# Kernel optimization log

Hardware: AMD Instinct MI355X
Metric: run time of the kernel (lower is better)

## Reference

```python
import jax, jax.numpy as jnp
import numpy as np

N = 100000      # hits
K = 256         # max truth objects per event
C = 2           # n_ccoords
NCLS = 6        # n_classes
Q_MIN = 0.5
S_B = 1.0
ENERGY_DEN_OFFSET = 1.0
PAYLOAD_BETA_CLIP = 0.1
USE_AVG_CC = 0.0
BETA_CLIP = 1.0 - 1e-5


def _divide_no_nan(num, den):
    return jnp.where(den == 0.0, 0.0, num / jnp.where(den == 0.0, 1.0, den))


def setup_inputs() -> dict:
    key = jax.random.key(0)
    ks = jax.random.split(key, 12)
    pred_beta = jax.random.uniform(ks[0], (N, 1), minval=0.01, maxval=0.99)
    pred_ccoords = jax.random.normal(ks[1], (N, C))
    pred_energy = jax.random.uniform(ks[2], (N, 1), minval=0.0, maxval=100.0)
    pred_pos = 50.0 * jax.random.normal(ks[3], (N, 2))
    pred_time = jax.random.normal(ks[4], (N, 1))
    pred_id = jax.random.normal(ks[5], (N, NCLS))
    t_energy = jax.random.uniform(ks[6], (N, 1), minval=0.1, maxval=100.0)
    t_pos = 50.0 * jax.random.normal(ks[7], (N, 2))
    t_time = jax.random.normal(ks[8], (N, 1))
    t_pid = jax.random.randint(ks[9], (N, 1), 1, NCLS + 1).astype(jnp.float32)
    t_idx = jax.random.randint(ks[10], (N, 1), -1, K)  # -1 == noise
    rowsplits = jnp.array([0, N], dtype=jnp.int32)
    return dict(pred_beta=pred_beta, pred_ccoords=pred_ccoords,
                pred_energy=pred_energy, pred_pos=pred_pos,
                pred_time=pred_time, pred_id=pred_id,
                t_energy=t_energy, t_pos=t_pos, t_time=t_time, t_pid=t_pid,
                t_idx=t_idx, rowsplits=rowsplits)


def oc_loss(pred_beta, pred_ccoords, pred_energy, pred_pos, pred_time,
            pred_id, t_energy, t_pos, t_time, t_pid, t_idx):
    beta = jnp.clip(pred_beta[:, 0], 0.0, BETA_CLIP)          # [N]
    q = jnp.arctanh(beta) ** 2 + Q_MIN                        # [N] charge
    tidx = t_idx[:, 0]
    not_noise = tidx >= 0                                     # [N]
    tclip = jnp.where(not_noise, tidx, 0)

    # hit->object assignment matrix [N, K]
    M = jax.nn.one_hot(tclip, K, dtype=beta.dtype) * not_noise[:, None].astype(beta.dtype)
    counts = M.sum(axis=0)                                    # [K]
    obj_valid = counts > 0.0
    n_valid = jnp.maximum(obj_valid.sum().astype(beta.dtype), 1.0)

    # condensation point per object: highest-beta hit of that object
    score = jnp.where(M > 0.0, beta[:, None], -1.0)           # [N, K]
    alpha = jnp.argmax(score, axis=0)                         # [K]
    x_alpha = pred_ccoords[alpha]                             # [K, C]
    mean_cc = (M.T @ pred_ccoords) / jnp.maximum(counts, 1.0)[:, None]
    x_k = USE_AVG_CC * mean_cc + (1.0 - USE_AVG_CC) * x_alpha
    q_alpha = q[alpha]                                        # [K]
    beta_alpha = beta[alpha]

    # pairwise hit <-> condensation-point squared distances [N, K]
    diff = pred_ccoords[:, None, :] - x_k[None, :, :]
    distsq = jnp.sum(diff * diff, axis=-1)

    qq = q[:, None] * q_alpha[None, :]                        # [N, K]
    # attractive potential: own-object hits pulled toward condensation point
    v_att_k = (M * distsq * qq).sum(axis=0) / jnp.maximum(counts, 1.0)
    V_att = jnp.where(obj_valid, v_att_k, 0.0).sum() / n_valid
    # repulsive potential: all other hits pushed out of a unit ball
    hinge = jax.nn.relu(1.0 - jnp.sqrt(distsq + 1e-6))
    v_rep_k = ((1.0 - M) * hinge * qq).sum(axis=0) / jnp.maximum(N - counts, 1.0)
    V_rep = jnp.where(obj_valid, v_rep_k, 0.0).sum() / n_valid

    # beta terms: sharpen condensation points, suppress noise beta
    L_beta = jnp.where(obj_valid, 1.0 - beta_alpha, 0.0).sum() / n_valid
    n_noise = jnp.maximum((~not_noise).astype(beta.dtype).sum(), 1.0)
    L_noise = S_B * jnp.where(not_noise, 0.0, beta).sum() / n_noise

    # --- per-hit payload losses ---
    ew = jax.nn.relu(jnp.where(t_energy > 10.0,
                               1.0, (t_energy - 0.5) / 10.0 * 10.0 / 9.5))
    e_loss = _divide_no_nan((t_energy - pred_energy) ** 2,
                            t_energy + ENERGY_DEN_OFFSET)
    p_loss = jnp.sum((t_pos - pred_pos) ** 2, axis=-1, keepdims=True) / 100.0
    tm_loss = (t_time - pred_time) ** 2
    cls_loss = 1e-8 * jnp.mean(pred_id ** 2, axis=-1, keepdims=True)
    payload = jnp.concatenate([e_loss, p_loss, tm_loss, cls_loss], axis=-1) * ew  # [N,4]
    payload = jnp.where(pred_beta < PAYLOAD_BETA_CLIP, 0.0, payload)

    # beta-weighted average of payload over each truth object
    pw = beta * not_noise.astype(beta.dtype)                  # [N]
    num = M.T @ (payload * pw[:, None])                       # [K, 4]
    den = (M * pw[:, None]).sum(axis=0)                       # [K]
    per_obj = num / jnp.maximum(den, 1e-6)[:, None]
    L_payload = (jnp.where(obj_valid[:, None], per_obj, 0.0).sum(axis=0) / n_valid).sum()

    return V_att + V_rep + L_beta + L_noise + L_payload


def reference(pred_beta, pred_ccoords, pred_energy, pred_pos, pred_time,
              pred_id, t_energy, t_pos, t_time, t_pid, t_idx, rowsplits):
    return oc_loss(pred_beta, pred_ccoords, pred_energy, pred_pos, pred_time,
                   pred_id, t_energy, t_pos, t_time, t_pid, t_idx)
```

## Files before the change

kernel.cpp:

```cpp
#include <hip/hip_runtime.h>
#include <hip/hip_bf16.h>
#include <math.h>

#define KOBJ 256
#define B1   256
#define NW   4
#define WSTR 257
#define QMIN 0.5f
#define BETA_CLIP_C (1.0f - 1e-5f)

typedef unsigned long long u64;

__global__ __launch_bounds__(256) void partials(
    const float*  __restrict__ pred_beta,
    const float*  __restrict__ pred_energy,
    const float2* __restrict__ pred_pos,
    const float*  __restrict__ pred_time,
    const float2* __restrict__ pred_id2,
    const float*  __restrict__ t_energy,
    const float2* __restrict__ t_pos,
    const float*  __restrict__ t_time,
    const int*    __restrict__ t_idx,
    u64*    __restrict__ pk_part,
    float*  __restrict__ cnt_part,
    float*  __restrict__ den_part,
    float*  __restrict__ num_part,
    float*  __restrict__ noise_part,
    int n)
{
    __shared__ u64   spk[NW][WSTR];
    __shared__ float scnt[NW][WSTR], sden[NW][WSTR], snum[NW][WSTR];
    __shared__ float snoise[256];
    int t = threadIdx.x;
    int b = blockIdx.x;
    int w = t >> 6;
    for (int i = t; i < NW * WSTR; i += 256) {
        ((u64*)spk)[i] = 0;
        ((float*)scnt)[i] = 0.f;
        ((float*)sden)[i] = 0.f;
        ((float*)snum)[i] = 0.f;
    }
    __syncthreads();

    float noise = 0.0f;
    for (int i = b * 256 + t; i < n; i += B1 * 256) {
        int tid = t_idx[i];
        float braw = pred_beta[i];
        float beta = fminf(fmaxf(braw, 0.0f), BETA_CLIP_C);
        if (tid >= 0) {
            atomicAdd(&scnt[w][tid], 1.0f);
            u64 key = ((u64)__float_as_uint(beta) << 32) |
                      (u64)(0x7FFFFFFFu - (unsigned)i);
            atomicMax(&spk[w][tid], key);
            float te = t_energy[i];
            float ew = (te > 10.0f) ? 1.0f : fmaxf(0.0f, (te - 0.5f) / 9.5f);
            float de = te - pred_energy[i];
            float el = de * de / (te + 1.0f);
            float2 tp = t_pos[i];
            float2 pp = pred_pos[i];
            float dpx = tp.x - pp.x, dpy = tp.y - pp.y;
            float pl = (dpx * dpx + dpy * dpy) * 0.01f;
            float dt = t_time[i] - pred_time[i];
            float tl = dt * dt;
            float2 id0 = pred_id2[3 * i];
            float2 id1 = pred_id2[3 * i + 1];
            float2 id2 = pred_id2[3 * i + 2];
            float cs = id0.x * id0.x + id0.y * id0.y + id1.x * id1.x +
                       id1.y * id1.y + id2.x * id2.x + id2.y * id2.y;
            cs *= (1e-8f / 6.0f);
            float mask = (braw < 0.1f) ? 0.0f : 1.0f;
            float wgt = mask * ew * beta;
            atomicAdd(&sden[w][tid], beta);
            atomicAdd(&snum[w][tid], (el + pl + tl + cs) * wgt);
        } else {
            noise += beta;
        }
    }
    __syncthreads();
    u64 pk = spk[0][t];
    { u64 q = spk[1][t]; if (q > pk) pk = q; }
    { u64 q = spk[2][t]; if (q > pk) pk = q; }
    { u64 q = spk[3][t]; if (q > pk) pk = q; }
    float cnt = scnt[0][t] + scnt[1][t] + scnt[2][t] + scnt[3][t];
    float den = sden[0][t] + sden[1][t] + sden[2][t] + sden[3][t];
    float num = snum[0][t] + snum[1][t] + snum[2][t] + snum[3][t];
    int o = t * B1 + b;
    pk_part[o]  = pk;
    cnt_part[o] = cnt;
    den_part[o] = den;
    num_part[o] = num;
    snoise[t] = noise;
    __syncthreads();
    for (int s = 128; s > 0; s >>= 1) {
        if (t < s) snoise[t] += snoise[t + s];
        __syncthreads();
    }
    if (t == 0) noise_part[b] = snoise[0];
}

__global__ __launch_bounds__(256) void merge(
    const float2* __restrict__ pred_ccoords,
    const u64*    __restrict__ pk_part,
    const float*  __restrict__ cnt_part,
    const float*  __restrict__ den_part,
    const float*  __restrict__ num_part,
    float4* __restrict__ objA,
    float4* __restrict__ objB)
{
    __shared__ u64   spk[256];
    __shared__ float scnt[256], sden[256], snum[256];
    int k = blockIdx.x;
    int b = threadIdx.x;
    int o = k * B1 + b;
    u64 pk = pk_part[o];
    float cnt = cnt_part[o];
    float den = den_part[o];
    float nsum = num_part[o];
    spk[b] = pk; scnt[b] = cnt; sden[b] = den; snum[b] = nsum;
    __syncthreads();
    for (int s = 128; s > 0; s >>= 1) {
        if (b < s) {
            u64 p = spk[b + s]; if (p > spk[b]) spk[b] = p;
            scnt[b] += scnt[b + s];
            sden[b] += sden[b + s];
            snum[b] += snum[b + s];
        }
        __syncthreads();
    }
    if (b == 0) {
        float cs = scnt[0];
        bool valid = cs > 0.f;
        float xk = 0.f, yk = 0.f, qa = 0.f, lb = 0.f, pay = 0.f;
        if (valid) {
            u64 p = spk[0];
            unsigned a = 0x7FFFFFFFu - (unsigned)(p & 0xFFFFFFFFull);
            float ba = __uint_as_float((unsigned)(p >> 32));
            float2 cc = pred_ccoords[a];
            xk = cc.x; yk = cc.y;
            float at = atanhf(ba);
            qa = at * at + QMIN;
            lb = 1.0f - ba;
            pay = snum[0] / fmaxf(sden[0], 1e-6f);
        }
        objA[k] = make_float4(xk, yk, qa, cs);
        objB[k] = make_float4(pay, lb, valid ? 1.f : 0.f, 0.f);
    }
}

__global__ __launch_bounds__(256) void heavy(
    const float*  __restrict__ pred_beta,
    const float2* __restrict__ pred_ccoords,
    const int*    __restrict__ t_idx,
    const float4* __restrict__ objA,
    float* __restrict__ rep_part,
    float* __restrict__ att_part,
    int n, int hstr)
{
    __shared__ float4 pts[256];
    int t = threadIdx.x;
    int p = blockIdx.x * 256 + t;
    float4 pt;
    if (p < n) {
        float beta = fminf(fmaxf(pred_beta[p], 0.0f), BETA_CLIP_C);
        float at = atanhf(beta);
        float2 cc = pred_ccoords[p];
        pt = make_float4(cc.x, cc.y, at * at + QMIN, __int_as_float(t_idx[p]));
    } else {
        pt = make_float4(0.f, 0.f, 0.f, __int_as_float(-2));
    }
    pts[t] = pt;
    float4 oa = objA[t];
    float xk = oa.x, yk = oa.y;
    __syncthreads();
    float rep = 0.f, att = 0.f;
    #pragma unroll 8
    for (int j = 0; j < 256; ++j) {
        float4 s = pts[j];
        float dx = s.x - xk, dy = s.y - yk;
        float d2 = fmaf(dy, dy, fmaf(dx, dx, 1e-6f));
        float r = __builtin_amdgcn_sqrtf(d2);
        float h = fmaxf(0.0f, 1.0f - r);
        bool own = (__float_as_int(s.w) == t);
        rep = fmaf(own ? 0.0f : h,  s.z, rep);
        att = fmaf(own ? d2 : 0.0f, s.z, att);
    }
    int o = t * hstr + blockIdx.x;
    rep_part[o] = rep;
    att_part[o] = att;
}

__global__ __launch_bounds__(256) void final1(
    const float4* __restrict__ objA,
    const float4* __restrict__ objB,
    const float*  __restrict__ rep_part,
    const float*  __restrict__ att_part,
    float4* __restrict__ objC,
    int n, int nbh, int hstr)
{
    __shared__ float srep[256], satt[256];
    int k = blockIdx.x;
    int b = threadIdx.x;
    float rep = 0.f, att = 0.f;
    int o = k * hstr + b;
    if (b < nbh)        { rep += rep_part[o];        att += att_part[o]; }
    if (b + 256 < nbh)  { rep += rep_part[o + 256];  att += att_part[o + 256]; }
    srep[b] = rep; satt[b] = att;
    __syncthreads();
    for (int s = 128; s > 0; s >>= 1) {
        if (b < s) { srep[b] += srep[b + s]; satt[b] += satt[b + s]; }
        __syncthreads();
    }
    if (b == 0) {
        float4 a  = objA[k];
        float4 b4 = objB[k];
        float cnt = a.w, qa = a.z, valid = b4.z;
        float vatt = valid * satt[0] * qa / fmaxf(cnt, 1.0f);
        float vrep = valid * srep[0] * qa / fmaxf((float)n - cnt, 1.0f);
        objC[k] = make_float4(vatt + vrep + b4.y + b4.x, valid, cnt, 0.f);
    }
}

__global__ __launch_bounds__(256) void final2(
    const float4* __restrict__ objC,
    const float*  __restrict__ noise_part,
    float* __restrict__ out, int n)
{
    __shared__ float4 sred[256];
    int t = threadIdx.x;
    float4 c = objC[t];
    c.w = noise_part[t];
    sred[t] = c;
    __syncthreads();
    for (int s = 128; s > 0; s >>= 1) {
        if (t < s) {
            float4 x = sred[t], y = sred[t + s];
            sred[t] = make_float4(x.x + y.x, x.y + y.y, x.z + y.z, x.w + y.w);
        }
        __syncthreads();
    }
    if (t == 0) {
        float4 r = sred[0];
        float nv = fmaxf(r.y, 1.0f);
        float nnoise = fmaxf((float)n - r.z, 1.0f);
        out[0] = r.x / nv + r.w / nnoise;
    }
}

extern "C" void kernel_launch(void* const* d_in, const int* in_sizes, int n_in,
                              void* d_out, int out_size, void* d_ws, size_t ws_size,
                              hipStream_t stream) {
    const float*  pred_beta    = (const float*)d_in[0];
    const float2* pred_ccoords = (const float2*)d_in[1];
    const float*  pred_energy  = (const float*)d_in[2];
    const float2* pred_pos     = (const float2*)d_in[3];
    const float*  pred_time    = (const float*)d_in[4];
    const float2* pred_id2     = (const float2*)d_in[5];
    const float*  t_energy     = (const float*)d_in[6];
    const float2* t_pos        = (const float2*)d_in[7];
    const float*  t_time       = (const float*)d_in[8];
    const int*    t_idx        = (const int*)d_in[10];
    int n = in_sizes[0];
    int nbh = (n + 255) / 256;
    int hstr = (nbh + 8) & ~7;

    char* base = (char*)d_ws;
    size_t off = 0;
    u64*    pk_part    = (u64*)   (base + off); off += (size_t)KOBJ * B1 * 8;
    float*  cnt_part   = (float*) (base + off); off += (size_t)KOBJ * B1 * 4;
    float*  den_part   = (float*) (base + off); off += (size_t)KOBJ * B1 * 4;
    float*  num_part   = (float*) (base + off); off += (size_t)KOBJ * B1 * 4;
    float*  noise_part = (float*) (base + off); off += 256 * 4;
    float4* objA       = (float4*)(base + off); off += KOBJ * 16;
    float4* objB       = (float4*)(base + off); off += KOBJ * 16;
    float4* objC       = (float4*)(base + off); off += KOBJ * 16;
    float*  rep_part   = (float*) (base + off); off += (size_t)KOBJ * hstr * 4;
    float*  att_part   = (float*) (base + off); off += (size_t)KOBJ * hstr * 4;

    partials<<<B1, 256, 0, stream>>>(pred_beta, pred_energy, pred_pos, pred_time,
                                     pred_id2, t_energy, t_pos, t_time, t_idx,
                                     pk_part, cnt_part, den_part, num_part, noise_part, n);
    merge<<<KOBJ, 256, 0, stream>>>(pred_ccoords, pk_part, cnt_part, den_part, num_part,
                                    objA, objB);
    heavy<<<nbh, 256, 0, stream>>>(pred_beta, pred_ccoords, t_idx, objA,
                                   rep_part, att_part, n, hstr);
    final1<<<KOBJ, 256, 0, stream>>>(objA, objB, rep_part, att_part, objC, n, nbh, hstr);
    final2<<<1, 256, 0, stream>>>(objC, noise_part, (float*)d_out, n);
}
```

Baseline: 105.0 us.

## Hoist own-object terms out of heavy loop and fuse final reductions

The heavy kernel's inner loop no longer tests ownership per pair. It accumulates the full hinge sum over all points, then subtracts each point's own-object contribution, computed once per point and added to shared memory with atomics; the attraction term comes only from that per-point path. Each block now processes 200 points instead of 256, which means more blocks. The two final kernels are merged into one, where the last-arriving block does the global reduction via a ticket counter, saving a launch. The subtraction can cause cancellation error, and the ticket scheme relies on fences and a counter reset inside the partials kernel.

```diff
diff --git a/kernel.cpp b/kernel.cpp
--- a/kernel.cpp
+++ b/kernel.cpp
@@ -1,11 +1,11 @@
 #include <hip/hip_runtime.h>
-#include <hip/hip_bf16.h>
 #include <math.h>
 
 #define KOBJ 256
 #define B1   256
 #define NW   4
 #define WSTR 257
+#define CHUNK 200
 #define QMIN 0.5f
 #define BETA_CLIP_C (1.0f - 1e-5f)
 
@@ -26,6 +26,7 @@
     float*  __restrict__ den_part,
     float*  __restrict__ num_part,
     float*  __restrict__ noise_part,
+    unsigned* __restrict__ tick,
     int n)
 {
     __shared__ u64   spk[NW][WSTR];
@@ -34,6 +35,7 @@
     int t = threadIdx.x;
     int b = blockIdx.x;
     int w = t >> 6;
+    if (b == 0 && t == 0) *tick = 0u;
     for (int i = t; i < NW * WSTR; i += 256) {
         ((u64*)spk)[i] = 0;
         ((float*)scnt)[i] = 0.f;
@@ -156,54 +158,74 @@
     float* __restrict__ att_part,
     int n, int hstr)
 {
-    __shared__ float4 pts[256];
+    __shared__ float4 pts[CHUNK];
+    __shared__ float corrR[KOBJ], corrA[KOBJ];
     int t = threadIdx.x;
-    int p = blockIdx.x * 256 + t;
-    float4 pt;
-    if (p < n) {
-        float beta = fminf(fmaxf(pred_beta[p], 0.0f), BETA_CLIP_C);
-        float at = atanhf(beta);
-        float2 cc = pred_ccoords[p];
-        pt = make_float4(cc.x, cc.y, at * at + QMIN, __int_as_float(t_idx[p]));
-    } else {
-        pt = make_float4(0.f, 0.f, 0.f, __int_as_float(-2));
-    }
-    pts[t] = pt;
+    corrR[t] = 0.f;
+    corrA[t] = 0.f;
+    float4 pt = make_float4(0.f, 0.f, 0.f, __int_as_float(-2));
+    int p = blockIdx.x * CHUNK + t;
+    if (t < CHUNK) {
+        if (p < n) {
+            float beta = fminf(fmaxf(pred_beta[p], 0.0f), BETA_CLIP_C);
+            float at = atanhf(beta);
+            float2 cc = pred_ccoords[p];
+            pt = make_float4(cc.x, cc.y, at * at + QMIN, __int_as_float(t_idx[p]));
+        }
+        pts[t] = pt;
+    }
     float4 oa = objA[t];
     float xk = oa.x, yk = oa.y;
     __syncthreads();
-    float rep = 0.f, att = 0.f;
+
+    int tid = __float_as_int(pt.w);
+    if (t < CHUNK && tid >= 0) {
+        float4 ok = objA[tid];
+        float dx = pt.x - ok.x, dy = pt.y - ok.y;
+        float d2 = fmaf(dy, dy, fmaf(dx, dx, 1e-6f));
+        float r = __builtin_amdgcn_sqrtf(d2);
+        float h = fmaxf(0.0f, 1.0f - r);
+        atomicAdd(&corrA[tid], d2 * pt.z);
+        atomicAdd(&corrR[tid], h * pt.z);
+    }
+
+    float rep = 0.f;
     #pragma unroll 8
-    for (int j = 0; j < 256; ++j) {
+    for (int j = 0; j < CHUNK; ++j) {
         float4 s = pts[j];
         float dx = s.x - xk, dy = s.y - yk;
         float d2 = fmaf(dy, dy, fmaf(dx, dx, 1e-6f));
         float r = __builtin_amdgcn_sqrtf(d2);
         float h = fmaxf(0.0f, 1.0f - r);
-        bool own = (__float_as_int(s.w) == t);
-        rep = fmaf(own ? 0.0f : h,  s.z, rep);
-        att = fmaf(own ? d2 : 0.0f, s.z, att);
-    }
+        rep = fmaf(h, s.z, rep);
+    }
+    __syncthreads();
     int o = t * hstr + blockIdx.x;
-    rep_part[o] = rep;
-    att_part[o] = att;
-}
-
-__global__ __launch_bounds__(256) void final1(
+    rep_part[o] = rep - corrR[t];
+    att_part[o] = corrA[t];
+}
+
+__global__ __launch_bounds__(256) void finalk(
     const float4* __restrict__ objA,
     const float4* __restrict__ objB,
     const float*  __restrict__ rep_part,
     const float*  __restrict__ att_part,
-    float4* __restrict__ objC,
+    const float*  __restrict__ noise_part,
+    float*    __restrict__ objCf,
+    unsigned* __restrict__ tick,
+    float*    __restrict__ out,
     int n, int nbh, int hstr)
 {
     __shared__ float srep[256], satt[256];
+    __shared__ float4 sred[256];
+    __shared__ int lastflag;
     int k = blockIdx.x;
     int b = threadIdx.x;
     float rep = 0.f, att = 0.f;
-    int o = k * hstr + b;
-    if (b < nbh)        { rep += rep_part[o];        att += att_part[o]; }
-    if (b + 256 < nbh)  { rep += rep_part[o + 256];  att += att_part[o + 256]; }
+    for (int j = b; j < nbh; j += 256) {
+        rep += rep_part[k * hstr + j];
+        att += att_part[k * hstr + j];
+    }
     srep[b] = rep; satt[b] = att;
     __syncthreads();
     for (int s = 128; s > 0; s >>= 1) {
@@ -216,33 +238,36 @@
         float cnt = a.w, qa = a.z, valid = b4.z;
         float vatt = valid * satt[0] * qa / fmaxf(cnt, 1.0f);
         float vrep = valid * srep[0] * qa / fmaxf((float)n - cnt, 1.0f);
-        objC[k] = make_float4(vatt + vrep + b4.y + b4.x, valid, cnt, 0.f);
-    }
-}
-
-__global__ __launch_bounds__(256) void final2(
-    const float4* __restrict__ objC,
-    const float*  __restrict__ noise_part,
-    float* __restrict__ out, int n)
-{
-    __shared__ float4 sred[256];
-    int t = threadIdx.x;
-    float4 c = objC[t];
-    c.w = noise_part[t];
-    sred[t] = c;
-    __syncthreads();
-    for (int s = 128; s > 0; s >>= 1) {
-        if (t < s) {
-            float4 x = sred[t], y = sred[t + s];
-            sred[t] = make_float4(x.x + y.x, x.y + y.y, x.z + y.z, x.w + y.w);
-        }
+        float s0 = vatt + vrep + b4.y + b4.x;
+        atomicExch(&objCf[4 * k + 0], s0);
+        atomicExch(&objCf[4 * k + 1], valid);
+        atomicExch(&objCf[4 * k + 2], cnt);
+        __threadfence();
+        unsigned prev = atomicAdd(tick, 1u);
+        lastflag = (prev == (unsigned)(KOBJ - 1)) ? 1 : 0;
+    }
+    __syncthreads();
+    if (lastflag) {
+        __threadfence();
+        float s0  = atomicAdd(&objCf[4 * b + 0], 0.0f);
+        float val = atomicAdd(&objCf[4 * b + 1], 0.0f);
+        float cnt = atomicAdd(&objCf[4 * b + 2], 0.0f);
+        float noi = noise_part[b];
+        sred[b] = make_float4(s0, val, cnt, noi);
         __syncthreads();
-    }
-    if (t == 0) {
-        float4 r = sred[0];
-        float nv = fmaxf(r.y, 1.0f);
-        float nnoise = fmaxf((float)n - r.z, 1.0f);
-        out[0] = r.x / nv + r.w / nnoise;
+        for (int s = 128; s > 0; s >>= 1) {
+            if (b < s) {
+                float4 x = sred[b], y = sred[b + s];
+                sred[b] = make_float4(x.x + y.x, x.y + y.y, x.z + y.z, x.w + y.w);
+            }
+            __syncthreads();
+        }
+        if (b == 0) {
+            float4 r = sred[0];
+            float nv = fmaxf(r.y, 1.0f);
+            float nnoise = fmaxf((float)n - r.z, 1.0f);
+            out[0] = r.x / nv + r.w / nnoise;
+        }
     }
 }
 
@@ -260,7 +285,7 @@
     const float*  t_time       = (const float*)d_in[8];
     const int*    t_idx        = (const int*)d_in[10];
     int n = in_sizes[0];
-    int nbh = (n + 255) / 256;
+    int nbh = (n + CHUNK - 1) / CHUNK;
     int hstr = (nbh + 8) & ~7;
 
     char* base = (char*)d_ws;
@@ -272,17 +297,19 @@
     float*  noise_part = (float*) (base + off); off += 256 * 4;
     float4* objA       = (float4*)(base + off); off += KOBJ * 16;
     float4* objB       = (float4*)(base + off); off += KOBJ * 16;
-    float4* objC       = (float4*)(base + off); off += KOBJ * 16;
+    float*  objCf      = (float*) (base + off); off += KOBJ * 4 * 4;
+    unsigned* tick     = (unsigned*)(base + off); off += 16;
     float*  rep_part   = (float*) (base + off); off += (size_t)KOBJ * hstr * 4;
     float*  att_part   = (float*) (base + off); off += (size_t)KOBJ * hstr * 4;
 
     partials<<<B1, 256, 0, stream>>>(pred_beta, pred_energy, pred_pos, pred_time,
                                      pred_id2, t_energy, t_pos, t_time, t_idx,
-                                     pk_part, cnt_part, den_part, num_part, noise_part, n);
+                                     pk_part, cnt_part, den_part, num_part, noise_part,
+                                     tick, n);
     merge<<<KOBJ, 256, 0, stream>>>(pred_ccoords, pk_part, cnt_part, den_part, num_part,
                                     objA, objB);
     heavy<<<nbh, 256, 0, stream>>>(pred_beta, pred_ccoords, t_idx, objA,
                                    rep_part, att_part, n, hstr);
-    final1<<<KOBJ, 256, 0, stream>>>(objA, objB, rep_part, att_part, objC, n, nbh, hstr);
-    final2<<<1, 256, 0, stream>>>(objC, noise_part, (float*)d_out, n);
-}
+    finalk<<<KOBJ, 256, 0, stream>>>(objA, objB, rep_part, att_part, noise_part,
+                                     objCf, tick, (float*)d_out, n, nbh, hstr);
+}
```

Result: slower. 107.3 us (+2.3%).
